# Performance work log

Measured on AMD Instinct MI355X. Metric: run time of the kernel, lower is better.

The kernel has to match this reference:

```python
import jax, jax.numpy as jnp
import numpy as np

N_NODES = 50000
N_EDGES = 400000
IN_DIM = 256
HID = 128
HEADS = 2
OUT_DIM = 64
LN_EPS = 1e-5
NEG_SLOPE = 0.2  # PyG GATConv default LeakyReLU slope


def _glorot(key, shape):
    fan = shape[0] if len(shape) == 1 else (np.prod(shape[:-1]) + shape[-1])
    s = float(np.sqrt(2.0 / fan))
    return jax.random.normal(key, shape, jnp.float32) * s


def setup_inputs() -> dict:
    key = jax.random.key(0)
    ks = jax.random.split(key, 32)
    inp = {}
    inp["X"] = jax.random.normal(ks[0], (N_NODES, IN_DIM), jnp.float32)
    inp["edge_index"] = jax.random.randint(ks[1], (2, N_EDGES), 0, N_NODES, dtype=jnp.int32)
    inp["edge_weight"] = jax.random.uniform(ks[2], (N_EDGES,), jnp.float32)
    dims = [(IN_DIM, HID), (HID, HID), (HID, HID)]
    k = 3
    for li, (din, dout) in enumerate(dims):
        inp[f"W{li}"] = _glorot(ks[k], (din, HEADS, dout)); k += 1
        inp[f"a_src{li}"] = _glorot(ks[k], (HEADS, dout)); k += 1
        inp[f"a_dst{li}"] = _glorot(ks[k], (HEADS, dout)); k += 1
        inp[f"b{li}"] = jnp.zeros((dout,), jnp.float32)
        inp[f"g{li}"] = jnp.ones((dout,), jnp.float32)
        inp[f"be{li}"] = jnp.zeros((dout,), jnp.float32)
    inp["Wout"] = _glorot(ks[k], (HID, OUT_DIM)); k += 1
    inp["bout"] = jnp.zeros((OUT_DIM,), jnp.float32)
    return inp


def _gat_layer(x, src, dst, n, W, a_s, a_d, b):
    # x: [n, din] -> h: [n, H, dout]
    h = jnp.einsum('ni,iho->nho', x, W)
    alpha_s = jnp.sum(h * a_s, axis=-1)  # [n, H]
    alpha_d = jnp.sum(h * a_d, axis=-1)  # [n, H]
    e = jax.nn.leaky_relu(alpha_s[src] + alpha_d[dst], NEG_SLOPE)  # [E, H]
    m = jax.ops.segment_max(e, dst, num_segments=n)               # [n, H]
    ex = jnp.exp(e - m[dst])
    denom = jax.ops.segment_sum(ex, dst, num_segments=n)          # [n, H]
    alpha = ex / (denom[dst] + 1e-16)                             # [E, H]
    out = jax.ops.segment_sum(alpha[:, :, None] * h[src], dst, num_segments=n)  # [n, H, dout]
    return jnp.mean(out, axis=1) + b  # concat=False -> head mean + bias


def _layernorm(x, g, be):
    mu = jnp.mean(x, axis=-1, keepdims=True)
    var = jnp.mean(jnp.square(x - mu), axis=-1, keepdims=True)
    return (x - mu) * jax.lax.rsqrt(var + LN_EPS) * g + be


def reference(X, edge_index, edge_weight,
              W0, a_src0, a_dst0, b0, g0, be0,
              W1, a_src1, a_dst1, b1, g1, be1,
              W2, a_src2, a_dst2, b2, g2, be2,
              Wout, bout):
    n = X.shape[0]
    vnode = jnp.mean(X, axis=0, keepdims=True)
    Xv = jnp.concatenate([X, vnode], axis=0)  # [n+1, din]
    nv = n + 1
    ar = jnp.arange(n, dtype=edge_index.dtype)
    full = jnp.full((n,), n, dtype=edge_index.dtype)
    loops = jnp.arange(nv, dtype=edge_index.dtype)  # PyG GATConv add_self_loops default
    src = jnp.concatenate([edge_index[0], ar, full, loops])
    dst = jnp.concatenate([edge_index[1], full, ar, loops])
    h = Xv
    params = [(W0, a_src0, a_dst0, b0, g0, be0),
              (W1, a_src1, a_dst1, b1, g1, be1),
              (W2, a_src2, a_dst2, b2, g2, be2)]
    for (W, a_s, a_d, b, g, be) in params:
        h = _gat_layer(h, src, dst, nv, W, a_s, a_d, b)
        h = _layernorm(h, g, be)
        h = jax.nn.gelu(h, approximate=False)  # torch nn.GELU default; dropout is eval-mode identity
    node = h[:-1]  # drop virtual node
    return node @ Wout + bout
```

## Files before the change

kernel.cpp:

```cpp
#include <hip/hip_runtime.h>
#include <cmath>
#include <climits>

#define DEV __device__ __forceinline__

constexpr int NN  = 50000;
constexpr int NE  = 400000;
constexpr int NV  = NN + 1;
constexpr int IND = 256;
constexpr int HD  = 128;
constexpr int NHC = 256;
constexpr int NBLK = (NN + 255) / 256;
constexpr int VB2  = (NN + 127) / 128;
constexpr int CB2  = (NE + 1023) / 1024;

typedef short short8 __attribute__((ext_vector_type(8)));
typedef float f32x4  __attribute__((ext_vector_type(4)));

DEV float lrelu(float x) { return x > 0.f ? x : 0.2f * x; }
DEV float gelu(float x)  { return x * 0.5f * (1.f + erff(x * 0.70710678118654752f)); }
DEV ushort f2bf(float f) { uint u = __float_as_uint(f); return (ushort)((u + 0x7FFFu + ((u >> 16) & 1u)) >> 16); }
DEV float  bf2f(ushort h) { return __uint_as_float((uint)h << 16); }
DEV float rlane_f(float v, int j) { return __uint_as_float(__builtin_amdgcn_readlane(__float_as_uint(v), j)); }

DEV void gload_lds16(const ushort* g, ushort* l) {
    __builtin_amdgcn_global_load_lds(
        (const __attribute__((address_space(1))) void*)g,
        (__attribute__((address_space(3))) void*)l,
        16, 0, 0);
}


__global__ __launch_bounds__(256) void vnode_count(const float* __restrict__ X,
                                                   ushort* __restrict__ Xv,
                                                   float* __restrict__ colsum,
                                                   const int* __restrict__ ei,
                                                   int* __restrict__ counts) {
    if (blockIdx.x < VB2) {
        __shared__ float cpart[4][256];
        int t = threadIdx.x;
        int w = t >> 6, l = t & 63;
        int r0 = blockIdx.x * 128 + w * 32;
        const float4* X4 = reinterpret_cast<const float4*>(X);
        ushort4*      Xv4 = reinterpret_cast<ushort4*>(Xv);
        float s0 = 0.f, s1 = 0.f, s2 = 0.f, s3 = 0.f;
        int rend = min(r0 + 32, NN);
        for (int r = r0; r < rend; ++r) {
            float4 v = X4[(size_t)r * 64 + l];
            ushort4 o = {f2bf(v.x), f2bf(v.y), f2bf(v.z), f2bf(v.w)};
            Xv4[(size_t)r * 64 + l] = o;
            s0 += v.x; s1 += v.y; s2 += v.z; s3 += v.w;
        }
        cpart[w][4 * l]     = s0;
        cpart[w][4 * l + 1] = s1;
        cpart[w][4 * l + 2] = s2;
        cpart[w][4 * l + 3] = s3;
        __syncthreads();
        float tot = cpart[0][t] + cpart[1][t] + cpart[2][t] + cpart[3][t];
        atomicAdd(&colsum[t], tot);
    } else {
        int e4 = (blockIdx.x - VB2) * 1024 + threadIdx.x * 4;
        if (e4 + 3 < NE) {
            int4 d = *reinterpret_cast<const int4*>(ei + NE + e4);
            atomicAdd(&counts[d.x], 1);
            atomicAdd(&counts[d.y], 1);
            atomicAdd(&counts[d.z], 1);
            atomicAdd(&counts[d.w], 1);
        } else {
            for (int j = e4; j < NE; ++j) atomicAdd(&counts[ei[NE + j]], 1);
        }
    }
}

__global__ __launch_bounds__(256) void scan1_kernel(const int* __restrict__ counts,
                                                    int* __restrict__ row_start,
                                                    int* __restrict__ blocksums) {
    __shared__ int s[256];
    int t = threadIdx.x, i = blockIdx.x * 256 + t;
    int v = (i < NN) ? counts[i] : 0;
    s[t] = v;
    __syncthreads();
    for (int off = 1; off < 256; off <<= 1) {
        int u = (t >= off) ? s[t - off] : 0;
        __syncthreads();
        s[t] += u;
        __syncthreads();
    }
    if (i < NN) row_start[i] = s[t] - v;
    if (t == 255) blocksums[blockIdx.x] = s[255];
}

__global__ __launch_bounds__(256) void scan2conv(const int* __restrict__ blocksums,
                                                 int* __restrict__ blockoffs,
                                                 const float* __restrict__ W0,
                                                 const float* __restrict__ W1,
                                                 const float* __restrict__ W2,
                                                 const float* __restrict__ Wout,
                                                 ushort* __restrict__ Wt0,
                                                 ushort* __restrict__ Wt1,
                                                 ushort* __restrict__ Wt2,
                                                 ushort* __restrict__ Wto,
                                                 const float* __restrict__ colsum,
                                                 ushort* __restrict__ Xv) {
    int t = threadIdx.x;
    if (blockIdx.x == 0) {
        __shared__ int s[256];
        int v = (t < NBLK) ? blocksums[t] : 0;
        s[t] = v;
        __syncthreads();
        for (int off = 1; off < 256; off <<= 1) {
            int u = (t >= off) ? s[t - off] : 0;
            __syncthreads();
            s[t] += u;
            __syncthreads();
        }
        if (t < NBLK) blockoffs[t] = s[t] - v;
        return;
    }
    int bid = blockIdx.x - 1;
    if (bid < 256) {
        int idx = bid * 256 + t;
        int k = idx >> 8, n = idx & 255;
        Wt0[n * IND + k] = f2bf(W0[idx]);
    } else if (bid < 384) {
        int idx = (bid - 256) * 256 + t;
        int k = idx >> 8, n = idx & 255;
        Wt1[n * HD + k] = f2bf(W1[idx]);
    } else if (bid < 512) {
        int idx = (bid - 384) * 256 + t;
        int k = idx >> 8, n = idx & 255;
        Wt2[n * HD + k] = f2bf(W2[idx]);
    } else if (bid < 544) {
        int idx = (bid - 512) * 256 + t;
        int k = idx >> 6, n = idx & 63;
        Wto[n * HD + k] = f2bf(Wout[idx]);
    } else {
        Xv[(size_t)NN * IND + t] = f2bf(colsum[t] * (1.0f / NN));
    }
}

__global__ __launch_bounds__(256) void scan3_kernel(int* __restrict__ row_start,
                                                    const int* __restrict__ blockoffs,
                                                    int* __restrict__ cursor) {
    int i = blockIdx.x * 256 + threadIdx.x;
    if (i < NN) {
        int r = row_start[i] + blockoffs[blockIdx.x];
        row_start[i] = r;
        cursor[i]    = r;
    }
    if (i == 0) row_start[NN] = NE;
}

__global__ __launch_bounds__(256) void fill_kernel(const int* __restrict__ ei,
                                                   int* __restrict__ cursor,
                                                   int* __restrict__ csr) {
    int e = blockIdx.x * 256 + threadIdx.x;
    if (e < NE) {
        int d   = ei[NE + e];
        int pos = atomicAdd(&cursor[d], 1);
        csr[pos] = ei[e];
    }
}


template <int K>
__global__ __launch_bounds__(256) void gemm_mfma(const ushort* __restrict__ A,
                                                 const ushort* __restrict__ Bt,
                                                 const float* __restrict__ a_s,
                                                 const float* __restrict__ a_d,
                                                 ushort* __restrict__ H,
                                                 float* __restrict__ as_,
                                                 float* __restrict__ ad_,
                                                 float* __restrict__ vacc,
                                                 float* __restrict__ vden) {
    __shared__ ushort Bs[256 * 32];
    if (blockIdx.x == 0) {
        vacc[threadIdx.x] = 0.f;
        if (threadIdx.x < 2) vden[threadIdx.x] = 0.f;
    }
    const int tid  = threadIdx.x;
    const int wave = tid >> 6, lane = tid & 63;
    const int wr   = wave >> 1, wc = wave & 1;
    const int lrow = lane & 15, lk = lane >> 4;
    const int r0   = blockIdx.x * 64 + wr * 32;

    int ar0 = min(r0 + lrow,      NV - 1);
    int ar1 = min(r0 + 16 + lrow, NV - 1);
    const ushort* Ap0 = A + (size_t)ar0 * K + lk * 8;
    const ushort* Ap1 = A + (size_t)ar1 * K + lk * 8;
    const int scol  = lane >> 2;
    const int sslot = lane & 3;

    f32x4 acc[2][8] = {};
    for (int k0 = 0; k0 < K; k0 += 32) {
#pragma unroll
        for (int q = 0; q < 4; ++q) {
            int cb = wave * 64 + q * 16;
            gload_lds16(Bt + (size_t)(cb + scol) * K + k0 + sslot * 8, &Bs[cb * 32]);
        }
        short8 a0 = *reinterpret_cast<const short8*>(Ap0 + k0);
        short8 a1 = *reinterpret_cast<const short8*>(Ap1 + k0);
        __syncthreads();
#pragma unroll
        for (int n = 0; n < 8; ++n) {
            short8 bf = *reinterpret_cast<const short8*>(&Bs[(wc * 128 + n * 16 + lrow) * 32 + lk * 8]);
            acc[0][n] = __builtin_amdgcn_mfma_f32_16x16x32_bf16(a0, bf, acc[0][n], 0, 0, 0);
            acc[1][n] = __builtin_amdgcn_mfma_f32_16x16x32_bf16(a1, bf, acc[1][n], 0, 0, 0);
        }
        __syncthreads();
    }

#pragma unroll
    for (int m = 0; m < 2; ++m)
#pragma unroll
        for (int n = 0; n < 8; ++n) {
            int c = wc * 128 + n * 16 + lrow;
#pragma unroll
            for (int r = 0; r < 4; ++r) {
                int row = r0 + m * 16 + lk * 4 + r;
                if (row < NV) H[(size_t)row * NHC + c] = f2bf(acc[m][n][r]);
            }
        }

    float cs[8], cd[8];
#pragma unroll
    for (int n = 0; n < 8; ++n) {
        cs[n] = a_s[wc * 128 + n * 16 + lrow];
        cd[n] = a_d[wc * 128 + n * 16 + lrow];
    }
#pragma unroll
    for (int m = 0; m < 2; ++m)
#pragma unroll
        for (int r = 0; r < 4; ++r) {
            float s = 0.f, d = 0.f;
#pragma unroll
            for (int n = 0; n < 8; ++n) {
                s += acc[m][n][r] * cs[n];
                d += acc[m][n][r] * cd[n];
            }
            for (int off = 1; off < 16; off <<= 1) {
                s += __shfl_xor(s, off);
                d += __shfl_xor(d, off);
            }
            int row = r0 + m * 16 + lk * 4 + r;
            if (lrow == 0 && row < NV) {
                as_[row * 2 + wc] = s;
                ad_[row * 2 + wc] = d;
            }
        }
}

__global__ __launch_bounds__(256) void vsum_kernel(const float* __restrict__ as_,
                                                   const float* __restrict__ ad_,
                                                   const ushort* __restrict__ H,
                                                   float* __restrict__ vden,
                                                   float* __restrict__ vacc) {
    __shared__ float w0s[64], w1s[64];
    __shared__ float part[4][256];
    int t = threadIdx.x;
    int w = t >> 6, l = t & 63;
    int r0 = blockIdx.x * 64;
    if (t < 64) {
        int r = r0 + t;
        float p0 = 0.f, p1 = 0.f;
        if (r < NV) {
            float2 adv = *reinterpret_cast<const float2*>(ad_ + 2 * NN);
            float2 asv = *reinterpret_cast<const float2*>(as_ + 2 * r);
            p0 = __expf(lrelu(asv.x + adv.x));
            p1 = __expf(lrelu(asv.y + adv.y));
        }
        w0s[t] = p0; w1s[t] = p1;
    }
    __syncthreads();
    const ushort4* H4 = reinterpret_cast<const ushort4*>(H);
    bool h0 = l < 32;
    float a0 = 0.f, a1 = 0.f, a2 = 0.f, a3 = 0.f;
    int rbase = r0 + w * 16;
#pragma unroll 4
    for (int it = 0; it < 16; ++it) {
        int r = rbase + it;
        if (r < NV) {
            float wt = h0 ? w0s[w * 16 + it] : w1s[w * 16 + it];
            ushort4 q = H4[(size_t)r * 64 + l];
            a0 += wt * bf2f(q.x); a1 += wt * bf2f(q.y);
            a2 += wt * bf2f(q.z); a3 += wt * bf2f(q.w);
        }
    }
    part[w][4 * l]     = a0;
    part[w][4 * l + 1] = a1;
    part[w][4 * l + 2] = a2;
    part[w][4 * l + 3] = a3;
    __syncthreads();
    float tot = part[0][t] + part[1][t] + part[2][t] + part[3][t];
    atomicAdd(&vacc[t], tot);
    if (t < 2) {
        const float* ws = t ? w1s : w0s;
        float d = 0.f;
        for (int j = 0; j < 64; ++j) d += ws[j];
        atomicAdd(&vden[t], d);
    }
}

__global__ __launch_bounds__(256) void node_kernel(const int* __restrict__ row_start,
                                                   const int* __restrict__ csr,
                                                   const float* __restrict__ as_,
                                                   const float* __restrict__ ad_,
                                                   const ushort* __restrict__ H,
                                                   const float* __restrict__ vacc,
                                                   const float* __restrict__ vden,
                                                   const float* __restrict__ b,
                                                   const float* __restrict__ g,
                                                   const float* __restrict__ be,
                                                   ushort* __restrict__ hn) {
    int wave = threadIdx.x >> 6, lane = threadIdx.x & 63;
    int i = blockIdx.x * 4 + wave;
    if (i > NN) return;
    int  l5 = lane & 31;
    bool h0 = lane < 32;

    float acc0 = 0.f, acc1 = 0.f, acc2 = 0.f, acc3 = 0.f, dp;
    if (i == NN) {
        int base = (h0 ? 0 : 128) + 4 * l5;
        acc0 = vacc[base];     acc1 = vacc[base + 1];
        acc2 = vacc[base + 2]; acc3 = vacc[base + 3];
        dp = vden[h0 ? 0 : 1];
    } else {
        int rs = row_start[i], cnt = row_start[i + 1] - rs;
        int tot = cnt + 2;
        float2 adv = *reinterpret_cast<const float2*>(ad_ + 2 * i);
        float dp0 = 0.f, dp1 = 0.f;
        const ushort4* H4 = reinterpret_cast<const ushort4*>(H);
        for (int bse = 0; bse < tot; bse += 64) {
            int idx = bse + lane;
            int src_l = 0; float p0_l = 0.f, p1_l = 0.f;
            if (idx < tot) {
                src_l = idx < cnt ? csr[rs + idx] : (idx == cnt ? NN : i);
                float2 asv = *reinterpret_cast<const float2*>(as_ + 2 * src_l);
                p0_l = __expf(lrelu(asv.x + adv.x));
                p1_l = __expf(lrelu(asv.y + adv.y));
                dp0 += p0_l; dp1 += p1_l;
            }
            int chunk = min(64, tot - bse);
            int j = 0;
            for (; j + 4 <= chunk; j += 4) {
                int sA = __builtin_amdgcn_readlane(src_l, j);
                int sB = __builtin_amdgcn_readlane(src_l, j + 1);
                int sC = __builtin_amdgcn_readlane(src_l, j + 2);
                int sD = __builtin_amdgcn_readlane(src_l, j + 3);
                ushort4 qA = H4[(size_t)sA * 64 + lane];
                ushort4 qB = H4[(size_t)sB * 64 + lane];
                ushort4 qC = H4[(size_t)sC * 64 + lane];
                ushort4 qD = H4[(size_t)sD * 64 + lane];
                float wA = h0 ? rlane_f(p0_l, j)     : rlane_f(p1_l, j);
                float wB = h0 ? rlane_f(p0_l, j + 1) : rlane_f(p1_l, j + 1);
                float wC = h0 ? rlane_f(p0_l, j + 2) : rlane_f(p1_l, j + 2);
                float wD = h0 ? rlane_f(p0_l, j + 3) : rlane_f(p1_l, j + 3);
                acc0 += wA * bf2f(qA.x); acc1 += wA * bf2f(qA.y);
                acc2 += wA * bf2f(qA.z); acc3 += wA * bf2f(qA.w);
                acc0 += wB * bf2f(qB.x); acc1 += wB * bf2f(qB.y);
                acc2 += wB * bf2f(qB.z); acc3 += wB * bf2f(qB.w);
                acc0 += wC * bf2f(qC.x); acc1 += wC * bf2f(qC.y);
                acc2 += wC * bf2f(qC.z); acc3 += wC * bf2f(qC.w);
                acc0 += wD * bf2f(qD.x); acc1 += wD * bf2f(qD.y);
                acc2 += wD * bf2f(qD.z); acc3 += wD * bf2f(qD.w);
            }
            for (; j < chunk; ++j) {
                int   s = __builtin_amdgcn_readlane(src_l, j);
                ushort4 q = H4[(size_t)s * 64 + lane];
                float w = h0 ? rlane_f(p0_l, j) : rlane_f(p1_l, j);
                acc0 += w * bf2f(q.x); acc1 += w * bf2f(q.y);
                acc2 += w * bf2f(q.z); acc3 += w * bf2f(q.w);
            }
        }
        for (int off = 32; off; off >>= 1) {
            dp0 += __shfl_xor(dp0, off);
            dp1 += __shfl_xor(dp1, off);
        }
        dp = h0 ? dp0 : dp1;
    }

    float r = 1.f / (dp + 1e-16f);
    float4 bv = reinterpret_cast<const float4*>(b)[l5];
    float z0 = acc0 * r, z1 = acc1 * r, z2 = acc2 * r, z3 = acc3 * r;
    float y0 = 0.5f * (z0 + __shfl_xor(z0, 32)) + bv.x;
    float y1 = 0.5f * (z1 + __shfl_xor(z1, 32)) + bv.y;
    float y2 = 0.5f * (z2 + __shfl_xor(z2, 32)) + bv.z;
    float y3 = 0.5f * (z3 + __shfl_xor(z3, 32)) + bv.w;
    float s = y0 + y1 + y2 + y3;
    for (int off = 32; off; off >>= 1) s += __shfl_xor(s, off);
    float mu = s * (1.f / 256.f);
    float c0 = y0 - mu, c1 = y1 - mu, c2 = y2 - mu, c3 = y3 - mu;
    float v = c0 * c0 + c1 * c1 + c2 * c2 + c3 * c3;
    for (int off = 32; off; off >>= 1) v += __shfl_xor(v, off);
    float rstd = rsqrtf(v * (1.f / 256.f) + 1e-5f);
    if (h0) {
        float4 gv  = reinterpret_cast<const float4*>(g)[l5];
        float4 bev = reinterpret_cast<const float4*>(be)[l5];
        ushort4 o;
        o.x = f2bf(gelu(c0 * rstd * gv.x + bev.x));
        o.y = f2bf(gelu(c1 * rstd * gv.y + bev.y));
        o.z = f2bf(gelu(c2 * rstd * gv.z + bev.z));
        o.w = f2bf(gelu(c3 * rstd * gv.w + bev.w));
        *reinterpret_cast<ushort4*>(&hn[(size_t)i * HD + 4 * l5]) = o;
    }
}

__global__ __launch_bounds__(256) void out_mfma(const ushort* __restrict__ A,
                                                const ushort* __restrict__ Bt,
                                                const float* __restrict__ bout,
                                                float* __restrict__ out) {
    __shared__ ushort Bs[64 * 32];
    const int tid  = threadIdx.x;
    const int wave = tid >> 6, lane = tid & 63;
    const int lrow = lane & 15, lk = lane >> 4;
    const int r0   = blockIdx.x * 128 + wave * 32;

    int ar0 = min(r0 + lrow,      NN - 1);
    int ar1 = min(r0 + 16 + lrow, NN - 1);
    const ushort* Ap0 = A + (size_t)ar0 * HD + lk * 8;
    const ushort* Ap1 = A + (size_t)ar1 * HD + lk * 8;
    const int scol  = lane >> 2;
    const int sslot = lane & 3;

    f32x4 acc[2][4] = {};
#pragma unroll
    for (int k0 = 0; k0 < HD; k0 += 32) {
        int cb = wave * 16;
        gload_lds16(Bt + (size_t)(cb + scol) * HD + k0 + sslot * 8, &Bs[cb * 32]);
        short8 a0 = *reinterpret_cast<const short8*>(Ap0 + k0);
        short8 a1 = *reinterpret_cast<const short8*>(Ap1 + k0);
        __syncthreads();
#pragma unroll
        for (int n = 0; n < 4; ++n) {
            short8 bf = *reinterpret_cast<const short8*>(&Bs[(n * 16 + lrow) * 32 + lk * 8]);
            acc[0][n] = __builtin_amdgcn_mfma_f32_16x16x32_bf16(a0, bf, acc[0][n], 0, 0, 0);
            acc[1][n] = __builtin_amdgcn_mfma_f32_16x16x32_bf16(a1, bf, acc[1][n], 0, 0, 0);
        }
        __syncthreads();
    }
#pragma unroll
    for (int m = 0; m < 2; ++m)
#pragma unroll
        for (int n = 0; n < 4; ++n) {
            int c = n * 16 + lrow;
            float bc = bout[c];
#pragma unroll
            for (int r = 0; r < 4; ++r) {
                int row = r0 + m * 16 + lk * 4 + r;
                if (row < NN) out[(size_t)row * 64 + c] = acc[m][n][r] + bc;
            }
        }
}


extern "C" void kernel_launch(void* const* d_in, const int* in_sizes, int n_in,
                              void* d_out, int out_size, void* d_ws, size_t ws_size,
                              hipStream_t stream) {
    (void)in_sizes; (void)n_in; (void)out_size; (void)ws_size;

    const float* X  = (const float*)d_in[0];
    const int*   ei = (const int*)d_in[1];
    const float* W[3]   = {(const float*)d_in[3],  (const float*)d_in[9],  (const float*)d_in[15]};
    const float* Asp[3] = {(const float*)d_in[4],  (const float*)d_in[10], (const float*)d_in[16]};
    const float* Adp[3] = {(const float*)d_in[5],  (const float*)d_in[11], (const float*)d_in[17]};
    const float* Bb[3]  = {(const float*)d_in[6],  (const float*)d_in[12], (const float*)d_in[18]};
    const float* Gg[3]  = {(const float*)d_in[7],  (const float*)d_in[13], (const float*)d_in[19]};
    const float* Be[3]  = {(const float*)d_in[8],  (const float*)d_in[14], (const float*)d_in[20]};
    const float* Wout = (const float*)d_in[21];
    const float* bout = (const float*)d_in[22];
    float* out = (float*)d_out;

    uintptr_t base = (uintptr_t)d_ws;
    auto take = [&](size_t bytes) {
        uintptr_t p = base;
        base += (bytes + 255) & ~(size_t)255;
        return p;
    };
    ushort* Xv    = (ushort*)take((size_t)NV * IND * 2);
    ushort* Hbuf  = (ushort*)take((size_t)NV * NHC * 2);
    ushort* hA    = (ushort*)take((size_t)NV * HD * 2);
    ushort* hB    = (ushort*)take((size_t)NV * HD * 2);
    ushort* Wt0   = (ushort*)take((size_t)256 * IND * 2);
    ushort* Wt1   = (ushort*)take((size_t)256 * HD * 2);
    ushort* Wt2   = (ushort*)take((size_t)256 * HD * 2);
    ushort* Wto   = (ushort*)take((size_t)64 * HD * 2);
    float* as_    = (float*)take((size_t)NV * 2 * 4);
    float* ad_    = (float*)take((size_t)NV * 2 * 4);
    float* colsum = (float*)take(256 * 4);
    int*   counts = (int*)take((size_t)NN * 4);
    int*   rowst  = (int*)take((size_t)(NN + 1) * 4);
    int*   cursor = (int*)take((size_t)NN * 4);
    int*   csr    = (int*)take((size_t)NE * 4);
    int*   bsums  = (int*)take((size_t)NBLK * 4);
    int*   boffs  = (int*)take((size_t)NBLK * 4);
    float* vden   = (float*)take(2 * 4);
    float* vacc   = (float*)take(256 * 4);
    ushort* Wt[3] = {Wt0, Wt1, Wt2};

    hipMemsetAsync(counts, 0, (size_t)NN * 4, stream);
    hipMemsetAsync(colsum, 0, 256 * 4, stream);
    vnode_count<<<VB2 + CB2, 256, 0, stream>>>(X, Xv, colsum, ei, counts);
    scan1_kernel<<<NBLK, 256, 0, stream>>>(counts, rowst, bsums);
    scan2conv<<<546, 256, 0, stream>>>(bsums, boffs, W[0], W[1], W[2], Wout,
                                       Wt0, Wt1, Wt2, Wto, colsum, Xv);
    scan3_kernel<<<NBLK, 256, 0, stream>>>(rowst, boffs, cursor);
    fill_kernel<<<(NE + 255) / 256, 256, 0, stream>>>(ei, cursor, csr);

    const ushort* hin = Xv;
    ushort* houts[3] = {hA, hB, hA};
    for (int li = 0; li < 3; ++li) {
        if (li == 0)
            gemm_mfma<IND><<<(NV + 63) / 64, 256, 0, stream>>>(hin, Wt[li], Asp[li], Adp[li], Hbuf, as_, ad_, vacc, vden);
        else
            gemm_mfma<HD><<<(NV + 63) / 64, 256, 0, stream>>>(hin, Wt[li], Asp[li], Adp[li], Hbuf, as_, ad_, vacc, vden);
        vsum_kernel<<<(NV + 63) / 64, 256, 0, stream>>>(as_, ad_, Hbuf, vden, vacc);
        node_kernel<<<NN / 4 + 1, 256, 0, stream>>>(rowst, csr, as_, ad_, Hbuf, vacc, vden,
                                                    Bb[li], Gg[li], Be[li], houts[li]);
        hin = houts[li];
    }
    out_mfma<<<(NN + 127) / 128, 256, 0, stream>>>(hin, Wto, bout, out);
}
```

Measured before the change: 480.9 us.

## Stage full-K weight tiles in swizzled LDS, enlarge GEMM blocks, use tanh GELU

The GEMM kernels now load a 128-wide K slab of the transposed weights into LDS once, with an XOR swizzle to avoid bank conflicts. This replaces the per-32-K async global_load_lds copies and the two barriers each step needed. The layer GEMM moves to 512-thread blocks covering 128 rows, and out_mfma loads its whole weight matrix once up front. GELU switches from exact erf to the tanh approximation with fast exp, which changes numerics slightly compared with the erf-based reference.

After: 458.0 us. -4.8%, faster.

```diff
diff --git a/kernel.cpp b/kernel.cpp
--- a/kernel.cpp
+++ b/kernel.cpp
@@ -18,17 +18,15 @@
 typedef float f32x4  __attribute__((ext_vector_type(4)));
 
 DEV float lrelu(float x) { return x > 0.f ? x : 0.2f * x; }
-DEV float gelu(float x)  { return x * 0.5f * (1.f + erff(x * 0.70710678118654752f)); }
+DEV float gelu(float x) {
+    float y = 0.7978845608028654f * (x + 0.044715f * x * x * x);
+    float e = __expf(2.f * y);
+    float t = (e - 1.f) * __frcp_rn(e + 1.f);
+    return 0.5f * x * (1.f + t);
+}
 DEV ushort f2bf(float f) { uint u = __float_as_uint(f); return (ushort)((u + 0x7FFFu + ((u >> 16) & 1u)) >> 16); }
 DEV float  bf2f(ushort h) { return __uint_as_float((uint)h << 16); }
 DEV float rlane_f(float v, int j) { return __uint_as_float(__builtin_amdgcn_readlane(__float_as_uint(v), j)); }
-
-DEV void gload_lds16(const ushort* g, ushort* l) {
-    __builtin_amdgcn_global_load_lds(
-        (const __attribute__((address_space(1))) void*)g,
-        (__attribute__((address_space(3))) void*)l,
-        16, 0, 0);
-}
 
 
 __global__ __launch_bounds__(256) void vnode_count(const float* __restrict__ X,
@@ -164,50 +162,56 @@
 
 
 template <int K>
-__global__ __launch_bounds__(256) void gemm_mfma(const ushort* __restrict__ A,
-                                                 const ushort* __restrict__ Bt,
-                                                 const float* __restrict__ a_s,
-                                                 const float* __restrict__ a_d,
-                                                 ushort* __restrict__ H,
-                                                 float* __restrict__ as_,
-                                                 float* __restrict__ ad_,
-                                                 float* __restrict__ vacc,
-                                                 float* __restrict__ vden) {
-    __shared__ ushort Bs[256 * 32];
+__global__ __launch_bounds__(512, 4) void gemm_mfma(const ushort* __restrict__ A,
+                                                    const ushort* __restrict__ Bt,
+                                                    const float* __restrict__ a_s,
+                                                    const float* __restrict__ a_d,
+                                                    ushort* __restrict__ H,
+                                                    float* __restrict__ as_,
+                                                    float* __restrict__ ad_,
+                                                    float* __restrict__ vacc,
+                                                    float* __restrict__ vden) {
+    __shared__ ushort Bs[256 * 128];
     if (blockIdx.x == 0) {
-        vacc[threadIdx.x] = 0.f;
+        if (threadIdx.x < 256) vacc[threadIdx.x] = 0.f;
         if (threadIdx.x < 2) vden[threadIdx.x] = 0.f;
     }
     const int tid  = threadIdx.x;
     const int wave = tid >> 6, lane = tid & 63;
     const int wr   = wave >> 1, wc = wave & 1;
     const int lrow = lane & 15, lk = lane >> 4;
-    const int r0   = blockIdx.x * 64 + wr * 32;
+    const int r0   = blockIdx.x * 128 + wr * 32;
 
     int ar0 = min(r0 + lrow,      NV - 1);
     int ar1 = min(r0 + 16 + lrow, NV - 1);
     const ushort* Ap0 = A + (size_t)ar0 * K + lk * 8;
     const ushort* Ap1 = A + (size_t)ar1 * K + lk * 8;
-    const int scol  = lane >> 2;
-    const int sslot = lane & 3;
 
     f32x4 acc[2][8] = {};
-    for (int k0 = 0; k0 < K; k0 += 32) {
-#pragma unroll
-        for (int q = 0; q < 4; ++q) {
-            int cb = wave * 64 + q * 16;
-            gload_lds16(Bt + (size_t)(cb + scol) * K + k0 + sslot * 8, &Bs[cb * 32]);
-        }
-        short8 a0 = *reinterpret_cast<const short8*>(Ap0 + k0);
-        short8 a1 = *reinterpret_cast<const short8*>(Ap1 + k0);
+#pragma unroll
+    for (int h = 0; h < K / 128; ++h) {
         __syncthreads();
 #pragma unroll
-        for (int n = 0; n < 8; ++n) {
-            short8 bf = *reinterpret_cast<const short8*>(&Bs[(wc * 128 + n * 16 + lrow) * 32 + lk * 8]);
-            acc[0][n] = __builtin_amdgcn_mfma_f32_16x16x32_bf16(a0, bf, acc[0][n], 0, 0, 0);
-            acc[1][n] = __builtin_amdgcn_mfma_f32_16x16x32_bf16(a1, bf, acc[1][n], 0, 0, 0);
+        for (int i = 0; i < 8; ++i) {
+            int chunkid = tid + i * 512;
+            int col = chunkid >> 4, c = chunkid & 15;
+            short8 v = *reinterpret_cast<const short8*>(Bt + (size_t)col * K + h * 128 + c * 8);
+            *reinterpret_cast<short8*>(&Bs[col * 128 + ((c ^ (col & 7)) << 3)]) = v;
         }
         __syncthreads();
+#pragma unroll
+        for (int k0 = 0; k0 < 128; k0 += 32) {
+            short8 a0 = *reinterpret_cast<const short8*>(Ap0 + h * 128 + k0);
+            short8 a1 = *reinterpret_cast<const short8*>(Ap1 + h * 128 + k0);
+#pragma unroll
+            for (int n = 0; n < 8; ++n) {
+                int col = wc * 128 + n * 16 + lrow;
+                int c   = ((k0 >> 3) + lk) ^ (col & 7);
+                short8 bf = *reinterpret_cast<const short8*>(&Bs[col * 128 + (c << 3)]);
+                acc[0][n] = __builtin_amdgcn_mfma_f32_16x16x32_bf16(a0, bf, acc[0][n], 0, 0, 0);
+                acc[1][n] = __builtin_amdgcn_mfma_f32_16x16x32_bf16(a1, bf, acc[1][n], 0, 0, 0);
+            }
+        }
     }
 
 #pragma unroll
@@ -409,34 +413,39 @@
                                                 const ushort* __restrict__ Bt,
                                                 const float* __restrict__ bout,
                                                 float* __restrict__ out) {
-    __shared__ ushort Bs[64 * 32];
+    __shared__ ushort Bs[64 * 128];
     const int tid  = threadIdx.x;
     const int wave = tid >> 6, lane = tid & 63;
     const int lrow = lane & 15, lk = lane >> 4;
     const int r0   = blockIdx.x * 128 + wave * 32;
 
+#pragma unroll
+    for (int i = 0; i < 4; ++i) {
+        int chunkid = tid + i * 256;
+        int col = chunkid >> 4, c = chunkid & 15;
+        short8 v = *reinterpret_cast<const short8*>(Bt + (size_t)col * HD + c * 8);
+        *reinterpret_cast<short8*>(&Bs[col * 128 + ((c ^ (col & 7)) << 3)]) = v;
+    }
+    __syncthreads();
+
     int ar0 = min(r0 + lrow,      NN - 1);
     int ar1 = min(r0 + 16 + lrow, NN - 1);
     const ushort* Ap0 = A + (size_t)ar0 * HD + lk * 8;
     const ushort* Ap1 = A + (size_t)ar1 * HD + lk * 8;
-    const int scol  = lane >> 2;
-    const int sslot = lane & 3;
 
     f32x4 acc[2][4] = {};
 #pragma unroll
     for (int k0 = 0; k0 < HD; k0 += 32) {
-        int cb = wave * 16;
-        gload_lds16(Bt + (size_t)(cb + scol) * HD + k0 + sslot * 8, &Bs[cb * 32]);
         short8 a0 = *reinterpret_cast<const short8*>(Ap0 + k0);
         short8 a1 = *reinterpret_cast<const short8*>(Ap1 + k0);
-        __syncthreads();
 #pragma unroll
         for (int n = 0; n < 4; ++n) {
-            short8 bf = *reinterpret_cast<const short8*>(&Bs[(n * 16 + lrow) * 32 + lk * 8]);
+            int col = n * 16 + lrow;
+            int c   = ((k0 >> 3) + lk) ^ (col & 7);
+            short8 bf = *reinterpret_cast<const short8*>(&Bs[col * 128 + (c << 3)]);
             acc[0][n] = __builtin_amdgcn_mfma_f32_16x16x32_bf16(a0, bf, acc[0][n], 0, 0, 0);
             acc[1][n] = __builtin_amdgcn_mfma_f32_16x16x32_bf16(a1, bf, acc[1][n], 0, 0, 0);
         }
-        __syncthreads();
     }
 #pragma unroll
     for (int m = 0; m < 2; ++m)
@@ -510,9 +519,9 @@
     ushort* houts[3] = {hA, hB, hA};
     for (int li = 0; li < 3; ++li) {
         if (li == 0)
-            gemm_mfma<IND><<<(NV + 63) / 64, 256, 0, stream>>>(hin, Wt[li], Asp[li], Adp[li], Hbuf, as_, ad_, vacc, vden);
+            gemm_mfma<IND><<<(NV + 127) / 128, 512, 0, stream>>>(hin, Wt[li], Asp[li], Adp[li], Hbuf, as_, ad_, vacc, vden);
         else
-            gemm_mfma<HD><<<(NV + 63) / 64, 256, 0, stream>>>(hin, Wt[li], Asp[li], Adp[li], Hbuf, as_, ad_, vacc, vden);
+            gemm_mfma<HD><<<(NV + 127) / 128, 512, 0, stream>>>(hin, Wt[li], Asp[li], Adp[li], Hbuf, as_, ad_, vacc, vden);
         vsum_kernel<<<(NV + 63) / 64, 256, 0, stream>>>(as_, ad_, Hbuf, vden, vacc);
         node_kernel<<<NN / 4 + 1, 256, 0, stream>>>(rowst, csr, as_, ad_, Hbuf, vacc, vden,
                                                     Bb[li], Gg[li], Be[li], houts[li]);
```
